# Performance work log

Measured on AMD Instinct MI355X. Metric: run time of the kernel, lower is better.

Reference implementation:

```python
import jax, jax.numpy as jnp
import numpy as np

H = 8          # heads
C = 128        # out_channels per head (hidden_dim)
EMB = 256      # embedding_dim
NG = 64        # number of graphs in batch
EPS_LN = 1e-5


def _layer_norm(x, g, b):
    mu = x.mean(-1, keepdims=True)
    var = ((x - mu) ** 2).mean(-1, keepdims=True)
    return (x - mu) * jax.lax.rsqrt(var + EPS_LN) * g + b


def _transformer_conv(x, src, dst, Wq, bq, Wk, bk, Wv, bv, Ws, bs, Wb):
    # PyG TransformerConv, heads=H, concat=False, beta=True, root_weight=True
    N = x.shape[0]
    q = (x @ Wq + bq).reshape(N, H, C)
    k = (x @ Wk + bk).reshape(N, H, C)
    v = (x @ Wv + bv).reshape(N, H, C)
    # per-edge attention logits: q_i . k_j / sqrt(C)   (i=dst, j=src)
    logits = jnp.einsum('ehc,ehc->eh', q[dst], k[src]) / jnp.sqrt(jnp.asarray(C, x.dtype))
    # segment softmax over incoming edges of each dst node
    m = jax.ops.segment_max(logits, dst, num_segments=N)
    m = jnp.where(jnp.isfinite(m), m, 0.0)
    ex = jnp.exp(logits - m[dst])
    den = jax.ops.segment_sum(ex, dst, num_segments=N)
    alpha = ex / (den[dst] + 1e-16)                      # [E,H]
    msg = alpha[:, :, None] * v[src]                     # [E,H,C]
    out = jax.ops.segment_sum(msg, dst, num_segments=N)  # [N,H,C]
    out = out.mean(axis=1)                               # concat=False -> head mean
    # beta-gated skip connection
    x_r = x @ Ws + bs                                    # [N,C]
    beta = jax.nn.sigmoid(jnp.concatenate([out, x_r, out - x_r], axis=-1) @ Wb)  # [N,1]
    return beta * x_r + (1.0 - beta) * out


def _lin(k, fan_in, fan_out, scale=None):
    s = scale if scale is not None else 1.0 / np.sqrt(fan_in)
    k1, k2 = jax.random.split(k)
    W = jax.random.uniform(k1, (fan_in, fan_out), jnp.float32, -s, s)
    b = jax.random.uniform(k2, (fan_out,), jnp.float32, -s, s)
    return W, b


def setup_inputs() -> dict:
    key = jax.random.key(0)
    ks = jax.random.split(key, 32)
    N, E, V = 50000, 400000, 10000
    inp = {
        'x': jax.random.randint(ks[0], (N,), 0, V, jnp.int32),
        'edge_index': jax.random.randint(ks[1], (2, E), 0, N, jnp.int32),
        'batch': jnp.sort(jax.random.randint(ks[2], (N,), 0, NG, jnp.int32)),
        'emb_w': jax.random.normal(ks[3], (V, EMB), jnp.float32),
    }
    ki = 4
    for l, din in enumerate([EMB, C]):
        Wq, bq = _lin(ks[ki], din, H * C); ki += 1
        Wk, bk = _lin(ks[ki], din, H * C); ki += 1
        Wv, bv = _lin(ks[ki], din, H * C); ki += 1
        Ws, bs = _lin(ks[ki], din, C); ki += 1
        Wb, _ = _lin(ks[ki], 3 * C, 1); ki += 1
        inp.update({f'Wq{l}': Wq, f'bq{l}': bq, f'Wk{l}': Wk, f'bk{l}': bk,
                    f'Wv{l}': Wv, f'bv{l}': bv, f'Ws{l}': Ws, f'bs{l}': bs,
                    f'Wb{l}': Wb, f'g{l}': jnp.ones((C,), jnp.float32),
                    f'be{l}': jnp.zeros((C,), jnp.float32)})
    Wc1, bc1 = _lin(ks[ki], C, C // 2); ki += 1
    Wc2, bc2 = _lin(ks[ki], C // 2, 1); ki += 1
    inp.update({'Wc1': Wc1, 'bc1': bc1, 'Wc2': Wc2, 'bc2': bc2})
    return inp


def reference(x, edge_index, batch, emb_w,
              Wq0, bq0, Wk0, bk0, Wv0, bv0, Ws0, bs0, Wb0, g0, be0,
              Wq1, bq1, Wk1, bk1, Wv1, bv1, Ws1, bs1, Wb1, g1, be1,
              Wc1, bc1, Wc2, bc2):
    src, dst = edge_index[0], edge_index[1]
    h = emb_w[x]                                           # [N, EMB]
    # layer 0 (no residual, per original `if i > 0`)
    h = _transformer_conv(h, src, dst, Wq0, bq0, Wk0, bk0, Wv0, bv0, Ws0, bs0, Wb0)
    h = jax.nn.relu(_layer_norm(h, g0, be0))               # dropout = identity (eval)
    # layer 1 (residual)
    res = h
    h = _transformer_conv(h, src, dst, Wq1, bq1, Wk1, bk1, Wv1, bv1, Ws1, bs1, Wb1)
    h = jax.nn.relu(_layer_norm(h + res, g1, be1))
    # global mean pool over graphs
    s = jax.ops.segment_sum(h, batch, num_segments=NG)     # [NG, C]
    cnt = jax.ops.segment_sum(jnp.ones((h.shape[0],), h.dtype), batch, num_segments=NG)
    pooled = s / jnp.maximum(cnt, 1.0)[:, None]
    # classifier MLP
    z = jax.nn.relu(pooled @ Wc1 + bc1)
    return z @ Wc2 + bc2                                   # [NG, 1]
```

## Files before the change

kernel.cpp:

```cpp
#include <hip/hip_runtime.h>
#include <math.h>

#define HEADS 8
#define CDIM 128
#define HC 1024
#define EMBD 256
#define NGRAPH 64
#define QSCALE 0.08838834764831845f

typedef unsigned short u16;
typedef short s8v __attribute__((ext_vector_type(8)));
typedef float f4v __attribute__((ext_vector_type(4)));

__device__ __forceinline__ float b2f(u16 u) {
  union { unsigned int i; float f; } v; v.i = ((unsigned int)u) << 16; return v.f;
}
__device__ __forceinline__ u16 f2b(float f) {
  union { float f; unsigned int i; } v; v.f = f;
  unsigned int i = v.i;
  unsigned int r = (i + 0x7FFFu + ((i >> 16) & 1u)) >> 16;
  return (u16)r;
}
__device__ __forceinline__ void dec8(uint4 u, float* f) {
  union { unsigned int i; float x; } a;
  a.i = u.x << 16;         f[0] = a.x;
  a.i = u.x & 0xffff0000u; f[1] = a.x;
  a.i = u.y << 16;         f[2] = a.x;
  a.i = u.y & 0xffff0000u; f[3] = a.x;
  a.i = u.z << 16;         f[4] = a.x;
  a.i = u.z & 0xffff0000u; f[5] = a.x;
  a.i = u.w << 16;         f[6] = a.x;
  a.i = u.w & 0xffff0000u; f[7] = a.x;
}

__global__ __launch_bounds__(256) void embed_kernel(
    const int* __restrict__ x, const float* __restrict__ emb,
    u16* __restrict__ h0, int N)
{
  int idx = blockIdx.x * 256 + threadIdx.x;
  if (idx >= N * (EMBD / 4)) return;
  int n = idx >> 6;
  int j = (idx & 63) * 4;
  int vid = x[n];
  float4 f = *(const float4*)&emb[(size_t)vid * EMBD + j];
  ushort4 u;
  u.x = f2b(f.x); u.y = f2b(f.y); u.z = f2b(f.z); u.w = f2b(f.w);
  *(ushort4*)&h0[(size_t)n * EMBD + j] = u;
}

__global__ __launch_bounds__(256) void transposeWs_tiled(
    const float* __restrict__ in, u16* __restrict__ out, int R)
{
  __shared__ u16 tile[64][66];
  int r0 = blockIdx.x * 64, c0 = blockIdx.y * 64;
  int t = threadIdx.x;
  int ci = t & 63, q4 = t >> 6;
#pragma unroll
  for (int ii = 0; ii < 16; ii++) {
    int r = q4 + ii * 4;
    tile[r][ci] = f2b(in[(size_t)(r0 + r) * CDIM + c0 + ci]);
  }
  __syncthreads();
  int rr = t & 63;
#pragma unroll
  for (int ii = 0; ii < 16; ii++) {
    int c = q4 + ii * 4;
    out[(size_t)(c0 + c) * R + r0 + rr] = tile[rr][c];
  }
}

__global__ __launch_bounds__(256) void build_qkvT_tiled(
    const float* __restrict__ Wq, const float* __restrict__ Wk, const float* __restrict__ Wv,
    u16* __restrict__ WT, int K, int hpc)
{
  __shared__ u16 tile[64][130];
  int rg0 = blockIdx.x * 128;
  int kk0 = blockIdx.y * 64;
  int chunkCols = hpc * 384;
  int chunk = rg0 / chunkCols;
  int within = rg0 - chunk * chunkCols;
  int head = chunk * hpc + within / 384;
  int sub = within % 384;
  int sect = sub >> 7;
  const float* W = (sect == 0) ? Wq : (sect == 1 ? Wk : Wv);
  float scale = (sect == 0) ? QSCALE : 1.0f;
  int cc0 = head * CDIM;
  int t = threadIdx.x;
  int ci = t & 127, k2 = t >> 7;
#pragma unroll
  for (int ii = 0; ii < 32; ii++) {
    int ki = k2 + ii * 2;
    tile[ki][ci] = f2b(W[(size_t)(kk0 + ki) * HC + cc0 + ci] * scale);
  }
  __syncthreads();
  int k = t & 63, r4 = t >> 6;
#pragma unroll
  for (int ii = 0; ii < 32; ii++) {
    int r = r4 + ii * 4;
    WT[(size_t)(rg0 + r) * K + kk0 + k] = tile[k][r];
  }
}
__global__ __launch_bounds__(256) void build_qkvb(
    const float* __restrict__ bq, const float* __restrict__ bk, const float* __restrict__ bv,
    float* __restrict__ bT, int hpc)
{
  int rg = blockIdx.x * 256 + threadIdx.x;
  if (rg >= 3 * HC) return;
  int chunkCols = hpc * 384;
  int chunk = rg / chunkCols;
  int within = rg - chunk * chunkCols;
  int head = chunk * hpc + within / 384;
  int sub = within % 384;
  int sect = sub >> 7;
  int cc = head * CDIM + (sub & 127);
  bT[rg] = (sect == 0) ? bq[cc] * QSCALE : (sect == 1 ? bk[cc] : bv[cc]);
}

__global__ __launch_bounds__(256) void deg_kernel(const int* __restrict__ ei, int* __restrict__ deg, int E) {
  int e = blockIdx.x * 256 + threadIdx.x;
  if (e < E) atomicAdd(&deg[ei[E + e]], 1);
}
__global__ __launch_bounds__(256) void scan1_kernel(const int* __restrict__ deg, int* __restrict__ row_ptr,
                                                    int* __restrict__ bsum, int N) {
  __shared__ int sb[256];
  int t = threadIdx.x, idx = blockIdx.x * 256 + t;
  int x = (idx < N) ? deg[idx] : 0;
  sb[t] = x; __syncthreads();
  for (int off = 1; off < 256; off <<= 1) {
    int y = (t >= off) ? sb[t - off] : 0;
    __syncthreads(); sb[t] += y; __syncthreads();
  }
  if (idx < N) row_ptr[idx + 1] = sb[t];
  if (t == 255) bsum[blockIdx.x] = sb[255];
  if (idx == 0) row_ptr[0] = 0;
}
__global__ __launch_bounds__(256) void scan2_kernel(int* __restrict__ bsum, int B) {
  __shared__ int sb[256];
  int t = threadIdx.x;
  int x = (t < B) ? bsum[t] : 0;
  sb[t] = x; __syncthreads();
  for (int off = 1; off < 256; off <<= 1) {
    int y = (t >= off) ? sb[t - off] : 0;
    __syncthreads(); sb[t] += y; __syncthreads();
  }
  if (t < B) bsum[t] = sb[t] - x;
}
__global__ __launch_bounds__(256) void scan3_kernel(int* __restrict__ row_ptr, const int* __restrict__ bsum, int N) {
  int idx = blockIdx.x * 256 + threadIdx.x;
  if (idx < N) row_ptr[idx + 1] += bsum[idx >> 8];
}
__global__ __launch_bounds__(256) void scatter_kernel(const int* __restrict__ ei,
                                                      const int* __restrict__ row_ptr,
                                                      int* __restrict__ fill, int* __restrict__ col, int E) {
  int e = blockIdx.x * 256 + threadIdx.x;
  if (e >= E) return;
  int d = ei[E + e];
  int pos = row_ptr[d] + atomicAdd(&fill[d], 1);
  col[pos] = ei[e];
}
__global__ void gb_kernel(const int* __restrict__ batch, int* __restrict__ gb, int N) {
  int g = threadIdx.x;
  if (g > NGRAPH) return;
  int lo = 0, hi = N;
  while (lo < hi) { int mid = (lo + hi) >> 1; if (batch[mid] < g) lo = mid + 1; else hi = mid; }
  gb[g] = lo;
}

template <int K>
__global__ __launch_bounds__(256, 2) void gemm_lds(
    const u16* __restrict__ A, const u16* __restrict__ BT,
    const float* __restrict__ bias, u16* __restrict__ outT,
    int M, int Ncol)
{
  const int LDK = K + 8;
  const int KS = K / 32;
  __shared__ __align__(16) u16 As[64 * LDK];
  int t = threadIdx.x, lane = t & 63, w = t >> 6;
  int q4 = lane >> 4, cn = lane & 15;
  int m0 = blockIdx.y * 64;
  int nt = blockIdx.x * 4 + w;
  bool wActive = nt * 64 < Ncol;

  if (m0 + 64 <= M) {
    const u16* Ablk = A + (size_t)m0 * K;
#pragma unroll
    for (int ii = 0; ii < K / 32; ii++) {
      int g = (ii * 256 + t) * 8;
      int r = g / K, c = g - r * K;
      *(uint4*)&As[r * LDK + c] = *(const uint4*)(Ablk + g);
    }
  } else {
#pragma unroll
    for (int ii = 0; ii < K / 32; ii++) {
      int g = (ii * 256 + t) * 8;
      int r = g / K, c = g - r * K;
      int gr = m0 + r; if (gr >= M) gr = M - 1;
      *(uint4*)&As[r * LDK + c] = *(const uint4*)(A + (size_t)gr * K + c);
    }
  }
  __syncthreads();

  if (!wActive) return;

  f4v acc[4][4] = {};
  const u16* bb = BT + ((size_t)nt * 64 + cn) * K + q4 * 8;
#pragma unroll
  for (int ks = 0; ks < KS; ks++) {
    s8v bf[4], af[4];
#pragma unroll
    for (int ni = 0; ni < 4; ni++)
      bf[ni] = *(const s8v*)(bb + (size_t)ni * 16 * K + ks * 32);
#pragma unroll
    for (int mi = 0; mi < 4; mi++)
      af[mi] = *(const s8v*)&As[(mi * 16 + cn) * LDK + ks * 32 + q4 * 8];
#pragma unroll
    for (int mi = 0; mi < 4; mi++)
#pragma unroll
      for (int ni = 0; ni < 4; ni++)
        acc[mi][ni] = __builtin_amdgcn_mfma_f32_16x16x32_bf16(af[mi], bf[ni], acc[mi][ni], 0, 0, 0);
  }

  u16* obase = outT + (size_t)nt * M * 64;
  float bv[4];
#pragma unroll
  for (int ni = 0; ni < 4; ni++) bv[ni] = bias[nt * 64 + ni * 16 + cn];
#pragma unroll
  for (int mi = 0; mi < 4; mi++) {
#pragma unroll
    for (int j = 0; j < 4; j++) {
      int gm = m0 + mi * 16 + q4 * 4 + j;
      if (gm < M) {
#pragma unroll
        for (int ni = 0; ni < 4; ni++)
          obase[(size_t)gm * 64 + ni * 16 + cn] = f2b(acc[mi][ni][j] + bv[ni]);
      }
    }
  }
}

template <int HPC>
__global__ __launch_bounds__(256) void attn_chunk_kernel(
    const u16* __restrict__ qkv,
    const int* __restrict__ row_ptr, const int* __restrict__ col,
    float* __restrict__ outacc, int N, int first)
{
  int t = threadIdx.x;
  int w = t >> 6, lane = t & 63;
  int g = lane >> 4, i = lane & 15;
  int n, j;
  if (HPC == 4)      { n = blockIdx.x;                 j = w; }
  else if (HPC == 2) { n = blockIdx.x * 2 + (w >> 1);  j = w & 1; }
  else               { n = blockIdx.x * 4 + w;         j = 0; }
  bool active = (HPC == 4) ? true : (n < N);

  int itile = i >> 3, ioff = (i & 7) * 8;
  const u16* qb = qkv + (size_t)(j * 6 + 0 + itile) * N * 64 + ioff;
  const u16* kb = qkv + (size_t)(j * 6 + 2 + itile) * N * 64 + ioff;
  const u16* vb = qkv + (size_t)(j * 6 + 4 + itile) * N * 64 + ioff;

  float acc[8] = {};
  float m = -INFINITY, l = 0.f;
  if (active) {
    float qf[8];
    dec8(*(const uint4*)(qb + (size_t)n * 64), qf);
    int e0 = row_ptr[n], e1 = row_ptr[n + 1];
    for (int eb = e0; eb < e1; eb += 4) {
      int eg = eb + g;
      bool val = eg < e1;
      int s = col[val ? eg : e1 - 1];
      uint4 ku = *(const uint4*)(kb + (size_t)s * 64);
      uint4 vu = *(const uint4*)(vb + (size_t)s * 64);
      float kf[8];
      dec8(ku, kf);
      float p = kf[0] * qf[0] + kf[1] * qf[1] + kf[2] * qf[2] + kf[3] * qf[3]
              + kf[4] * qf[4] + kf[5] * qf[5] + kf[6] * qf[6] + kf[7] * qf[7];
      p += __shfl_xor(p, 1); p += __shfl_xor(p, 2);
      p += __shfl_xor(p, 4); p += __shfl_xor(p, 8);
      if (!val) p = -INFINITY;
      float pm = fmaxf(p, __shfl_xor(p, 16));
      pm = fmaxf(pm, __shfl_xor(pm, 32));
      float nm = fmaxf(m, pm);
      float al = __expf(m - nm);
      float pe = __expf(p - nm);
      float ps = pe + __shfl_xor(pe, 16);
      ps += __shfl_xor(ps, 32);
      l = l * al + ps;
      m = nm;
      float vf[8];
      dec8(vu, vf);
#pragma unroll
      for (int z = 0; z < 8; z++) acc[z] = acc[z] * al + pe * vf[z];
    }
  }
  float inv = 0.125f / (l + 1e-16f);
#pragma unroll
  for (int z = 0; z < 8; z++) {
    float a = acc[z] * inv;
    a += __shfl_xor(a, 16);
    a += __shfl_xor(a, 32);
    acc[z] = a;
  }

  if (HPC == 1) {
    if (active && g == 0) {
      float* op = outacc + (size_t)n * CDIM + i * 8;
      if (first) {
        *(float4*)op       = make_float4(acc[0], acc[1], acc[2], acc[3]);
        *(float4*)(op + 4) = make_float4(acc[4], acc[5], acc[6], acc[7]);
      } else {
        float4 o0 = *(float4*)op, o1 = *(float4*)(op + 4);
        *(float4*)op       = make_float4(o0.x + acc[0], o0.y + acc[1], o0.z + acc[2], o0.w + acc[3]);
        *(float4*)(op + 4) = make_float4(o1.x + acc[4], o1.y + acc[5], o1.z + acc[6], o1.w + acc[7]);
      }
    }
  } else {
    __shared__ float sacc[4][128];
    if (g == 0) {
      *(float4*)&sacc[w][i * 8]     = make_float4(acc[0], acc[1], acc[2], acc[3]);
      *(float4*)&sacc[w][i * 8 + 4] = make_float4(acc[4], acc[5], acc[6], acc[7]);
    }
    __syncthreads();
    if (HPC == 4) {
      if (t < 128) {
        float v = sacc[0][t] + sacc[1][t] + sacc[2][t] + sacc[3][t];
        size_t o = (size_t)blockIdx.x * CDIM + t;
        outacc[o] = first ? v : (outacc[o] + v);
      }
    } else {
      int nn = blockIdx.x * 2 + (t >> 7);
      int c = t & 127;
      if (nn < N) {
        float v = sacc[(t >> 7) * 2][c] + sacc[(t >> 7) * 2 + 1][c];
        size_t o = (size_t)nn * CDIM + c;
        outacc[o] = first ? v : (outacc[o] + v);
      }
    }
  }
}

template <int LAYER>
__global__ __launch_bounds__(256) void epilogue_kernel(
    const float* __restrict__ outacc, const u16* __restrict__ xrT,
    const float* __restrict__ Wb, const float* __restrict__ gam, const float* __restrict__ bet,
    const u16* __restrict__ res,
    u16* __restrict__ hout,
    float* __restrict__ houtf,
    int N)
{
  int t = threadIdx.x;
  int local = t >> 7, c = t & 127, w = t >> 6;
  int n = blockIdx.x * 2 + local;
  bool act = n < N;
  __shared__ float sred[8];
  __shared__ float smv[2][3];

  float oc = 0.f, xc = 0.f;
  if (act) {
    oc = outacc[(size_t)n * CDIM + c];
    xc = b2f(xrT[((size_t)(c >> 6) * N + n) * 64 + (c & 63)]);
  }
  float pb = oc * Wb[c] + xc * Wb[CDIM + c] + (oc - xc) * Wb[2 * CDIM + c];
#pragma unroll
  for (int off = 32; off; off >>= 1) pb += __shfl_down(pb, off, 64);
  if ((t & 63) == 0) sred[w] = pb;
  __syncthreads();
  if (t == 0)   smv[0][0] = 1.f / (1.f + __expf(-(sred[0] + sred[1])));
  if (t == 128) smv[1][0] = 1.f / (1.f + __expf(-(sred[2] + sred[3])));
  __syncthreads();
  float beta = smv[local][0];
  float val = beta * xc + (1.f - beta) * oc;
  if (LAYER == 1 && act) val += b2f(res[(size_t)n * CDIM + c]);

  float s1 = val, s2 = val * val;
#pragma unroll
  for (int off = 32; off; off >>= 1) {
    s1 += __shfl_down(s1, off, 64);
    s2 += __shfl_down(s2, off, 64);
  }
  __syncthreads();
  if ((t & 63) == 0) { sred[w * 2] = s1; sred[w * 2 + 1] = s2; }
  __syncthreads();
  if (t == 0) {
    float S1 = sred[0] + sred[2], S2 = sred[1] + sred[3];
    float mu = S1 * (1.f / CDIM);
    float var = fmaxf(S2 * (1.f / CDIM) - mu * mu, 0.f);
    smv[0][1] = mu; smv[0][2] = 1.f / sqrtf(var + 1e-5f);
  }
  if (t == 128) {
    float S1 = sred[4] + sred[6], S2 = sred[5] + sred[7];
    float mu = S1 * (1.f / CDIM);
    float var = fmaxf(S2 * (1.f / CDIM) - mu * mu, 0.f);
    smv[1][1] = mu; smv[1][2] = 1.f / sqrtf(var + 1e-5f);
  }
  __syncthreads();
  if (act) {
    float y = (val - smv[local][1]) * smv[local][2] * gam[c] + bet[c];
    y = fmaxf(y, 0.f);
    if (LAYER == 0) hout[(size_t)n * CDIM + c] = f2b(y);
    else            houtf[(size_t)n * CDIM + c] = y;
  }
}

__global__ __launch_bounds__(256) void classifier_kernel(
    const float* __restrict__ hf, const int* __restrict__ gb,
    const float* __restrict__ Wc1, const float* __restrict__ bc1,
    const float* __restrict__ Wc2, const float* __restrict__ bc2,
    float* __restrict__ out)
{
  int g = blockIdx.x, t = threadIdx.x;
  int half = t >> 7, c = t & 127;
  int s = gb[g], e = gb[g + 1];
  float acc = 0.f;
  for (int n = s + half; n < e; n += 2) acc += hf[(size_t)n * CDIM + c];
  __shared__ float sb[2][128];
  __shared__ float sp[128], sz[64];
  sb[half][c] = acc;
  __syncthreads();
  float cg = fmaxf((float)(e - s), 1.f);
  if (t < 128) sp[t] = (sb[0][t] + sb[1][t]) / cg;
  __syncthreads();
  if (t < 64) {
    float a = bc1[t];
    for (int cc = 0; cc < 128; cc++) a += sp[cc] * Wc1[cc * 64 + t];
    sz[t] = fmaxf(a, 0.f);
  }
  __syncthreads();
  if (t < 64) {
    float pbv = sz[t] * Wc2[t];
    for (int off = 32; off; off >>= 1) pbv += __shfl_down(pbv, off, 64);
    if (t == 0) out[g] = pbv + bc2[0];
  }
}

extern "C" void kernel_launch(void* const* d_in, const int* in_sizes, int n_in,
                              void* d_out, int out_size, void* d_ws, size_t ws_size,
                              hipStream_t stream)
{
  if (n_in != 30) return;

  const int N = in_sizes[0];
  const int E = in_sizes[1] / 2;

  const int* x     = (const int*)d_in[0];
  const int* ei    = (const int*)d_in[1];
  const int* batch = (const int*)d_in[2];
  const float* emb = (const float*)d_in[3];
  const float* Wq0 = (const float*)d_in[4];  const float* bq0 = (const float*)d_in[5];
  const float* Wk0 = (const float*)d_in[6];  const float* bk0 = (const float*)d_in[7];
  const float* Wv0 = (const float*)d_in[8];  const float* bv0 = (const float*)d_in[9];
  const float* Ws0 = (const float*)d_in[10]; const float* bs0 = (const float*)d_in[11];
  const float* Wb0 = (const float*)d_in[12]; const float* g0  = (const float*)d_in[13]; const float* be0 = (const float*)d_in[14];
  const float* Wq1 = (const float*)d_in[15]; const float* bq1 = (const float*)d_in[16];
  const float* Wk1 = (const float*)d_in[17]; const float* bk1 = (const float*)d_in[18];
  const float* Wv1 = (const float*)d_in[19]; const float* bv1 = (const float*)d_in[20];
  const float* Ws1 = (const float*)d_in[21]; const float* bs1 = (const float*)d_in[22];
  const float* Wb1 = (const float*)d_in[23]; const float* g1  = (const float*)d_in[24]; const float* be1 = (const float*)d_in[25];
  const float* Wc1 = (const float*)d_in[26]; const float* bc1 = (const float*)d_in[27];
  const float* Wc2 = (const float*)d_in[28]; const float* bc2 = (const float*)d_in[29];

  auto rnd = [](size_t b) { return (b + 511) & ~(size_t)511; };
  size_t fixedBytes =
      rnd((size_t)N * CDIM * 4) +
      rnd((size_t)N * EMBD * 2) +
      rnd((size_t)N * CDIM * 2) * 2 +
      rnd((size_t)3 * HC * EMBD * 2) +
      rnd((size_t)3 * HC * CDIM * 2) +
      rnd((size_t)3 * HC * 4) * 2 +
      rnd((size_t)CDIM * EMBD * 2) +
      rnd((size_t)CDIM * CDIM * 2) +
      rnd((size_t)N * 4) * 2 +
      rnd((size_t)(N + 1) * 4) +
      rnd((size_t)E * 4) +
      rnd(256 * 4) +
      rnd(65 * 4);
  int hpc = 1;
  if (ws_size >= fixedBytes + rnd((size_t)N * 4 * 384 * 2)) hpc = 4;
  else if (ws_size >= fixedBytes + rnd((size_t)N * 2 * 384 * 2)) hpc = 2;
  const int chunkCols = hpc * 384;
  const int nchunks = HEADS / hpc;

  char* ws = (char*)d_ws;
  size_t off = 0;
  auto alloc = [&](size_t bytes) -> void* {
    void* p = ws + off;
    off += (bytes + 511) & ~(size_t)511;
    return p;
  };
  u16*   qkvc  = (u16*)  alloc((size_t)N * chunkCols * 2);
  float* outacc= (float*)alloc((size_t)N * CDIM * 4);
  u16*   h0    = (u16*)  alloc((size_t)N * EMBD * 2);
  u16*   h1    = (u16*)  alloc((size_t)N * CDIM * 2);
  u16*   xrb   = (u16*)  alloc((size_t)N * CDIM * 2);
  u16*   WT0   = (u16*)  alloc((size_t)3 * HC * EMBD * 2);
  u16*   WT1   = (u16*)  alloc((size_t)3 * HC * CDIM * 2);
  float* bT0   = (float*)alloc((size_t)3 * HC * 4);
  float* bT1   = (float*)alloc((size_t)3 * HC * 4);
  u16*   WsT0  = (u16*)  alloc((size_t)CDIM * EMBD * 2);
  u16*   WsT1  = (u16*)  alloc((size_t)CDIM * CDIM * 2);
  int*   deg   = (int*)  alloc((size_t)N * 4);
  int*   fill  = (int*)  alloc((size_t)N * 4);
  int*   rowp  = (int*)  alloc((size_t)(N + 1) * 4);
  int*   colb  = (int*)  alloc((size_t)E * 4);
  int*   bsum  = (int*)  alloc(256 * 4);
  int*   gb    = (int*)  alloc(65 * 4);

  hipMemsetAsync(deg, 0, (size_t)N * 4, stream);
  hipMemsetAsync(fill, 0, (size_t)N * 4, stream);

  embed_kernel<<<(N * 64 + 255) / 256, 256, 0, stream>>>(x, emb, h0, N);
  { dim3 gT(3 * HC / 128, EMBD / 64);
    build_qkvT_tiled<<<gT, 256, 0, stream>>>(Wq0, Wk0, Wv0, WT0, EMBD, hpc); }
  { dim3 gT(3 * HC / 128, CDIM / 64);
    build_qkvT_tiled<<<gT, 256, 0, stream>>>(Wq1, Wk1, Wv1, WT1, CDIM, hpc); }
  build_qkvb<<<(3 * HC + 255) / 256, 256, 0, stream>>>(bq0, bk0, bv0, bT0, hpc);
  build_qkvb<<<(3 * HC + 255) / 256, 256, 0, stream>>>(bq1, bk1, bv1, bT1, hpc);
  { dim3 gT(EMBD / 64, CDIM / 64);
    transposeWs_tiled<<<gT, 256, 0, stream>>>(Ws0, WsT0, EMBD); }
  { dim3 gT(CDIM / 64, CDIM / 64);
    transposeWs_tiled<<<gT, 256, 0, stream>>>(Ws1, WsT1, CDIM); }

  int nb = (N + 255) / 256;
  deg_kernel<<<(E + 255) / 256, 256, 0, stream>>>(ei, deg, E);
  scan1_kernel<<<nb, 256, 0, stream>>>(deg, rowp, bsum, N);
  scan2_kernel<<<1, 256, 0, stream>>>(bsum, nb);
  scan3_kernel<<<nb, 256, 0, stream>>>(rowp, bsum, N);
  scatter_kernel<<<(E + 255) / 256, 256, 0, stream>>>(ei, rowp, fill, colb, E);
  gb_kernel<<<1, 128, 0, stream>>>(batch, gb, N);

  int rowStrips = (N + 63) / 64;
  int attnBlocks = (hpc == 4) ? N : (hpc == 2 ? (N + 1) / 2 : (N + 3) / 4);
  int epiBlocks = (N + 1) / 2;

  for (int layer = 0; layer < 2; layer++) {
    const u16* Ain   = (layer == 0) ? h0 : h1;
    const u16* WT    = (layer == 0) ? WT0 : WT1;
    const float* bT  = (layer == 0) ? bT0 : bT1;
    const u16* WsT   = (layer == 0) ? WsT0 : WsT1;
    const float* bs  = (layer == 0) ? bs0 : bs1;
    const float* Wb  = (layer == 0) ? Wb0 : Wb1;
    const float* gam = (layer == 0) ? g0 : g1;
    const float* bet = (layer == 0) ? be0 : be1;
    int K = (layer == 0) ? EMBD : CDIM;

    dim3 gXR(1, rowStrips);
    dim3 gQKV(chunkCols / 256, rowStrips);
    if (K == EMBD) gemm_lds<EMBD><<<gXR, 256, 0, stream>>>(Ain, WsT, bs, xrb, N, CDIM);
    else           gemm_lds<CDIM><<<gXR, 256, 0, stream>>>(Ain, WsT, bs, xrb, N, CDIM);
    for (int c = 0; c < nchunks; c++) {
      if (K == EMBD)
        gemm_lds<EMBD><<<gQKV, 256, 0, stream>>>(Ain, WT + (size_t)c * chunkCols * K,
                                                 bT + c * chunkCols, qkvc, N, chunkCols);
      else
        gemm_lds<CDIM><<<gQKV, 256, 0, stream>>>(Ain, WT + (size_t)c * chunkCols * K,
                                                 bT + c * chunkCols, qkvc, N, chunkCols);
      int first = (c == 0) ? 1 : 0;
      if (hpc == 4)      attn_chunk_kernel<4><<<attnBlocks, 256, 0, stream>>>(qkvc, rowp, colb, outacc, N, first);
      else if (hpc == 2) attn_chunk_kernel<2><<<attnBlocks, 256, 0, stream>>>(qkvc, rowp, colb, outacc, N, first);
      else               attn_chunk_kernel<1><<<attnBlocks, 256, 0, stream>>>(qkvc, rowp, colb, outacc, N, first);
    }
    if (layer == 0) {
      epilogue_kernel<0><<<epiBlocks, 256, 0, stream>>>(outacc, xrb, Wb, gam, bet,
                                                        (const u16*)nullptr, h1, (float*)nullptr, N);
    } else {
      epilogue_kernel<1><<<epiBlocks, 256, 0, stream>>>(outacc, xrb, Wb, gam, bet,
                                                        h1, (u16*)nullptr, (float*)qkvc, N);
    }
  }

  classifier_kernel<<<NGRAPH, 256, 0, stream>>>((const float*)qkvc, gb, Wc1, bc1, Wc2, bc2,
                                                (float*)d_out);
}
```

Before: 1.254 ms.

## Store QKV in fp16, use fdot2 logits and exp2 softmax with 2-edge unroll

The QKV GEMM now writes fp16 instead of bf16. Q is prescaled by log2(e)/sqrt(C) so the attention kernel can use exp2f, and the q·k logits are computed with packed fp16 fdot2 instructions. The edge loop handles two edge groups per iteration so more gathers are in flight, and the running-max rescale is applied only when the max grows. This targets decode ALU work and gather latency in the attention kernel, at the cost of fp16 range limits on Q, K and V. It also leaves an unused stub helper behind.

```diff
diff --git a/kernel.cpp b/kernel.cpp
--- a/kernel.cpp
+++ b/kernel.cpp
@@ -1,4 +1,5 @@
 #include <hip/hip_runtime.h>
+#include <hip/hip_fp16.h>
 #include <math.h>
 
 #define HEADS 8
@@ -7,10 +8,12 @@
 #define EMBD 256
 #define NGRAPH 64
 #define QSCALE 0.08838834764831845f
+#define QSCALE2 0.12751744f
 
 typedef unsigned short u16;
 typedef short s8v __attribute__((ext_vector_type(8)));
 typedef float f4v __attribute__((ext_vector_type(4)));
+typedef _Float16 h2v __attribute__((ext_vector_type(2)));
 
 __device__ __forceinline__ float b2f(u16 u) {
   union { unsigned int i; float f; } v; v.i = ((unsigned int)u) << 16; return v.f;
@@ -21,16 +24,16 @@
   unsigned int r = (i + 0x7FFFu + ((i >> 16) & 1u)) >> 16;
   return (u16)r;
 }
-__device__ __forceinline__ void dec8(uint4 u, float* f) {
-  union { unsigned int i; float x; } a;
-  a.i = u.x << 16;         f[0] = a.x;
-  a.i = u.x & 0xffff0000u; f[1] = a.x;
-  a.i = u.y << 16;         f[2] = a.x;
-  a.i = u.y & 0xffff0000u; f[3] = a.x;
-  a.i = u.z << 16;         f[4] = a.x;
-  a.i = u.z & 0xffff0000u; f[5] = a.x;
-  a.i = u.w << 16;         f[6] = a.x;
-  a.i = u.w & 0xffff0000u; f[7] = a.x;
+__device__ __forceinline__ u16 f2h(float f) {
+  __half h = __float2half(f);
+  return *(u16*)&h;
+}
+
+union U4H { uint4 u; h2v h[4]; };
+
+__device__ __forceinline__ float dot8h(uint4 ku, uint4 qu0, uint4 qu1) {
+  (void)qu1;
+  return 0.f;
 }
 
 __global__ __launch_bounds__(256) void embed_kernel(
@@ -83,7 +86,7 @@
   int sub = within % 384;
   int sect = sub >> 7;
   const float* W = (sect == 0) ? Wq : (sect == 1 ? Wk : Wv);
-  float scale = (sect == 0) ? QSCALE : 1.0f;
+  float scale = (sect == 0) ? QSCALE2 : 1.0f;
   int cc0 = head * CDIM;
   int t = threadIdx.x;
   int ci = t & 127, k2 = t >> 7;
@@ -113,7 +116,7 @@
   int sub = within % 384;
   int sect = sub >> 7;
   int cc = head * CDIM + (sub & 127);
-  bT[rg] = (sect == 0) ? bq[cc] * QSCALE : (sect == 1 ? bk[cc] : bv[cc]);
+  bT[rg] = (sect == 0) ? bq[cc] * QSCALE2 : (sect == 1 ? bk[cc] : bv[cc]);
 }
 
 __global__ __launch_bounds__(256) void deg_kernel(const int* __restrict__ ei, int* __restrict__ deg, int E) {
@@ -166,7 +169,7 @@
   gb[g] = lo;
 }
 
-template <int K>
+template <int K, int F16OUT>
 __global__ __launch_bounds__(256, 2) void gemm_lds(
     const u16* __restrict__ A, const u16* __restrict__ BT,
     const float* __restrict__ bias, u16* __restrict__ outT,
@@ -231,8 +234,10 @@
       int gm = m0 + mi * 16 + q4 * 4 + j;
       if (gm < M) {
 #pragma unroll
-        for (int ni = 0; ni < 4; ni++)
-          obase[(size_t)gm * 64 + ni * 16 + cn] = f2b(acc[mi][ni][j] + bv[ni]);
+        for (int ni = 0; ni < 4; ni++) {
+          float val = acc[mi][ni][j] + bv[ni];
+          obase[(size_t)gm * 64 + ni * 16 + cn] = F16OUT ? f2h(val) : f2b(val);
+        }
       }
     }
   }
@@ -261,35 +266,85 @@
   float acc[8] = {};
   float m = -INFINITY, l = 0.f;
   if (active) {
-    float qf[8];
-    dec8(*(const uint4*)(qb + (size_t)n * 64), qf);
+    U4H qu; qu.u = *(const uint4*)(qb + (size_t)n * 64);
     int e0 = row_ptr[n], e1 = row_ptr[n + 1];
-    for (int eb = e0; eb < e1; eb += 4) {
-      int eg = eb + g;
-      bool val = eg < e1;
-      int s = col[val ? eg : e1 - 1];
-      uint4 ku = *(const uint4*)(kb + (size_t)s * 64);
-      uint4 vu = *(const uint4*)(vb + (size_t)s * 64);
-      float kf[8];
-      dec8(ku, kf);
-      float p = kf[0] * qf[0] + kf[1] * qf[1] + kf[2] * qf[2] + kf[3] * qf[3]
-              + kf[4] * qf[4] + kf[5] * qf[5] + kf[6] * qf[6] + kf[7] * qf[7];
-      p += __shfl_xor(p, 1); p += __shfl_xor(p, 2);
-      p += __shfl_xor(p, 4); p += __shfl_xor(p, 8);
-      if (!val) p = -INFINITY;
-      float pm = fmaxf(p, __shfl_xor(p, 16));
-      pm = fmaxf(pm, __shfl_xor(pm, 32));
-      float nm = fmaxf(m, pm);
-      float al = __expf(m - nm);
-      float pe = __expf(p - nm);
-      float ps = pe + __shfl_xor(pe, 16);
-      ps += __shfl_xor(ps, 32);
-      l = l * al + ps;
-      m = nm;
-      float vf[8];
-      dec8(vu, vf);
-#pragma unroll
-      for (int z = 0; z < 8; z++) acc[z] = acc[z] * al + pe * vf[z];
+    for (int eb = e0; eb < e1; eb += 8) {
+      int egA = eb + g, egB = eb + 4 + g;
+      bool vA = egA < e1, vB = egB < e1;
+      int sA = col[vA ? egA : e1 - 1];
+      int sB = col[vB ? egB : e1 - 1];
+      U4H kuA, vuA, kuB, vuB;
+      kuA.u = *(const uint4*)(kb + (size_t)sA * 64);
+      kuB.u = *(const uint4*)(kb + (size_t)sB * 64);
+      vuA.u = *(const uint4*)(vb + (size_t)sA * 64);
+      vuB.u = *(const uint4*)(vb + (size_t)sB * 64);
+
+      float pA, pB;
+#if defined(__has_builtin) && __has_builtin(__builtin_amdgcn_fdot2)
+      pA = __builtin_amdgcn_fdot2(kuA.h[0], qu.h[0], 0.f, false);
+      pA = __builtin_amdgcn_fdot2(kuA.h[1], qu.h[1], pA, false);
+      pA = __builtin_amdgcn_fdot2(kuA.h[2], qu.h[2], pA, false);
+      pA = __builtin_amdgcn_fdot2(kuA.h[3], qu.h[3], pA, false);
+      pB = __builtin_amdgcn_fdot2(kuB.h[0], qu.h[0], 0.f, false);
+      pB = __builtin_amdgcn_fdot2(kuB.h[1], qu.h[1], pB, false);
+      pB = __builtin_amdgcn_fdot2(kuB.h[2], qu.h[2], pB, false);
+      pB = __builtin_amdgcn_fdot2(kuB.h[3], qu.h[3], pB, false);
+#else
+      pA = 0.f; pB = 0.f;
+#pragma unroll
+      for (int z = 0; z < 4; z++) {
+        pA += (float)kuA.h[z][0] * (float)qu.h[z][0] + (float)kuA.h[z][1] * (float)qu.h[z][1];
+        pB += (float)kuB.h[z][0] * (float)qu.h[z][0] + (float)kuB.h[z][1] * (float)qu.h[z][1];
+      }
+#endif
+#pragma unroll
+      for (int off = 1; off <= 8; off <<= 1) {
+        pA += __shfl_xor(pA, off, 64);
+        pB += __shfl_xor(pB, off, 64);
+      }
+      if (!vA) pA = -INFINITY;
+      if (!vB) pB = -INFINITY;
+
+      {
+        float pm = fmaxf(pA, __shfl_xor(pA, 16));
+        pm = fmaxf(pm, __shfl_xor(pm, 32));
+        if (pm > m) {
+          float al = exp2f(m - pm);
+          l *= al;
+#pragma unroll
+          for (int z = 0; z < 8; z++) acc[z] *= al;
+          m = pm;
+        }
+        float pe = exp2f(pA - m);
+        float ps = pe + __shfl_xor(pe, 16);
+        ps += __shfl_xor(ps, 32);
+        l += ps;
+#pragma unroll
+        for (int z = 0; z < 4; z++) {
+          acc[2 * z]     = fmaf(pe, (float)vuA.h[z][0], acc[2 * z]);
+          acc[2 * z + 1] = fmaf(pe, (float)vuA.h[z][1], acc[2 * z + 1]);
+        }
+      }
+      {
+        float pm = fmaxf(pB, __shfl_xor(pB, 16));
+        pm = fmaxf(pm, __shfl_xor(pm, 32));
+        if (pm > m) {
+          float al = exp2f(m - pm);
+          l *= al;
+#pragma unroll
+          for (int z = 0; z < 8; z++) acc[z] *= al;
+          m = pm;
+        }
+        float pe = exp2f(pB - m);
+        float ps = pe + __shfl_xor(pe, 16);
+        ps += __shfl_xor(ps, 32);
+        l += ps;
+#pragma unroll
+        for (int z = 0; z < 4; z++) {
+          acc[2 * z]     = fmaf(pe, (float)vuB.h[z][0], acc[2 * z]);
+          acc[2 * z + 1] = fmaf(pe, (float)vuB.h[z][1], acc[2 * z + 1]);
+        }
+      }
     }
   }
   float inv = 0.125f / (l + 1e-16f);
@@ -544,15 +599,15 @@
 
     dim3 gXR(1, rowStrips);
     dim3 gQKV(chunkCols / 256, rowStrips);
-    if (K == EMBD) gemm_lds<EMBD><<<gXR, 256, 0, stream>>>(Ain, WsT, bs, xrb, N, CDIM);
-    else           gemm_lds<CDIM><<<gXR, 256, 0, stream>>>(Ain, WsT, bs, xrb, N, CDIM);
+    if (K == EMBD) gemm_lds<EMBD, 0><<<gXR, 256, 0, stream>>>(Ain, WsT, bs, xrb, N, CDIM);
+    else           gemm_lds<CDIM, 0><<<gXR, 256, 0, stream>>>(Ain, WsT, bs, xrb, N, CDIM);
     for (int c = 0; c < nchunks; c++) {
       if (K == EMBD)
-        gemm_lds<EMBD><<<gQKV, 256, 0, stream>>>(Ain, WT + (size_t)c * chunkCols * K,
-                                                 bT + c * chunkCols, qkvc, N, chunkCols);
+        gemm_lds<EMBD, 1><<<gQKV, 256, 0, stream>>>(Ain, WT + (size_t)c * chunkCols * K,
+                                                    bT + c * chunkCols, qkvc, N, chunkCols);
       else
-        gemm_lds<CDIM><<<gQKV, 256, 0, stream>>>(Ain, WT + (size_t)c * chunkCols * K,
-                                                 bT + c * chunkCols, qkvc, N, chunkCols);
+        gemm_lds<CDIM, 1><<<gQKV, 256, 0, stream>>>(Ain, WT + (size_t)c * chunkCols * K,
+                                                    bT + c * chunkCols, qkvc, N, chunkCols);
       int first = (c == 0) ? 1 : 0;
       if (hpc == 4)      attn_chunk_kernel<4><<<attnBlocks, 256, 0, stream>>>(qkvc, rowp, colb, outacc, N, first);
       else if (hpc == 2) attn_chunk_kernel<2><<<attnBlocks, 256, 0, stream>>>(qkvc, rowp, colb, outacc, N, first);
```

Result: no change. 1.251 ms (-0.3%).
